# Kernel tuning notes

Measured on AMD Instinct MI355X. Metric: run time of the kernel, lower is better.

Reference implementation:

```python
import jax, jax.numpy as jnp
import numpy as np

TOP_K = 2
SCALING = 2.0  # LoRA alpha/rank scaling


def setup_inputs() -> dict:
    key = jax.random.key(0)
    ks = jax.random.split(key, 10)
    B, S, H, I, E, R = 1, 512, 2048, 1024, 8, 16
    w = 1.0 / np.sqrt(H)
    inp = {
        "x": jax.random.normal(ks[0], (B, S, H), jnp.float32),
        "gate_weight": jax.random.normal(ks[1], (E, H), jnp.float32) * w,
        "gate_lora_A": jax.random.normal(ks[2], (R, H), jnp.float32) * 0.02,
        "gate_lora_B": jax.random.normal(ks[3], (E, R), jnp.float32) * 0.02,
        "gate_up_proj": jax.random.normal(ks[4], (E, H, 2 * I), jnp.float32) * w,
        "down_proj": jax.random.normal(ks[5], (E, I, H), jnp.float32) * (1.0 / np.sqrt(I)),
        "gup_lora_A": jax.random.normal(ks[6], (E, R, H), jnp.float32) * 0.02,
        "gup_lora_B": jax.random.normal(ks[7], (E, 2 * I, R), jnp.float32) * 0.02,
        "down_lora_A": jax.random.normal(ks[8], (E, R, I), jnp.float32) * 0.02,
        "down_lora_B": jax.random.normal(ks[9], (E, H, R), jnp.float32) * 0.02,
    }
    return inp


def reference(x, gate_weight, gate_lora_A, gate_lora_B, gate_up_proj, down_proj,
              gup_lora_A, gup_lora_B, down_lora_A, down_lora_B):
    B, S, H = x.shape
    xf = x.reshape(-1, H)  # [T, H]

    # ---- router (base weight + LoRA delta) ----
    gate_delta = SCALING * (gate_lora_B @ gate_lora_A)  # [E, H]
    router_logits = xf @ gate_weight.T + xf @ gate_delta.T  # [T, E]
    probs = jax.nn.softmax(router_logits.astype(jnp.float32), axis=-1)
    routing_weights, selected = jax.lax.top_k(probs, TOP_K)  # [T, K]
    routing_weights = routing_weights / routing_weights.sum(-1, keepdims=True)  # norm_topk_prob
    routing_weights = routing_weights.astype(xf.dtype)

    # ---- expert MLP: compute all experts, combine top-k ----
    # (math identical to sparse scatter/grouped-GEMM dispatch for selected experts)
    gup = jnp.einsum('th,eho->teo', xf, gate_up_proj)  # [T, E, 2I]
    gup = gup + SCALING * jnp.einsum('ter,eor->teo',
                                     jnp.einsum('th,erh->ter', xf, gup_lora_A),
                                     gup_lora_B)
    gates, h = jnp.split(gup, 2, axis=-1)
    h = jax.nn.silu(gates) * h  # [T, E, I]

    out = jnp.einsum('tei,eih->teh', h, down_proj)  # [T, E, H]
    out = out + SCALING * jnp.einsum('ter,ehr->teh',
                                     jnp.einsum('tei,eri->ter', h, down_lora_A),
                                     down_lora_B)

    # gather the top-k expert outputs and combine with routing weights
    out_sel = jnp.take_along_axis(out, selected[:, :, None], axis=1)  # [T, K, H]
    y = jnp.einsum('tkh,tk->th', out_sel, routing_weights)
    return y.reshape(B, S, H)
```

## Files before the change

### kernel.cpp

```cpp
#include <hip/hip_runtime.h>


typedef short  s16x8 __attribute__((ext_vector_type(8)));
typedef float  f32x4 __attribute__((ext_vector_type(4)));
typedef unsigned short u16x8 __attribute__((ext_vector_type(8)));

__device__ __forceinline__ unsigned short f2bf(float f) {
  unsigned u = __builtin_bit_cast(unsigned, f);
  u += 0x7fffu + ((u >> 16) & 1u);
  return (unsigned short)(u >> 16);
}

#define PIPE_BARRIER() asm volatile("s_waitcnt lgkmcnt(0)\n\ts_barrier" ::: "memory")

#define OFF_CNT    0u
#define OFF_TER1A  256u
#define OFF_TER2   262400u
#define ZERO_SPAN  327936u
#define OFF_LIST   327936u
#define OFF_PW     344320u
#define OFF_WG     348416u
#define OFF_XBF    413952u
#define OFF_H      2511104u
#define OFF_OSEL   4608256u

__global__ void k_gatecomb(const float* __restrict__ gw, const float* __restrict__ gA,
                           const float* __restrict__ gB, float* __restrict__ Wg) {
  int idx = blockIdx.x * 256 + threadIdx.x;
  int e = idx >> 11, h = idx & 2047;
  float acc = gw[idx];
#pragma unroll
  for (int r = 0; r < 16; ++r)
    acc += 2.0f * gB[e * 16 + r] * gA[r * 2048 + h];
  Wg[idx] = acc;
}

__global__ void k_router(const float* __restrict__ x, const float* __restrict__ Wg,
                         int* __restrict__ cnt, int* __restrict__ list,
                         float* __restrict__ pw, unsigned short* __restrict__ xbf) {
  int t = blockIdx.x, tid = threadIdx.x;
  __shared__ float xs[2048];
  __shared__ float logits[8];
  for (int i = tid; i < 2048; i += 256) xs[i] = x[(size_t)t * 2048 + i];
  __syncthreads();
  {
    u16x8 o;
#pragma unroll
    for (int j = 0; j < 8; ++j) o[j] = f2bf(xs[tid * 8 + j]);
    *(u16x8*)(xbf + (size_t)t * 2048 + tid * 8) = o;
  }
  int e = tid >> 5, l = tid & 31;
  float s = 0.f;
  for (int h = l; h < 2048; h += 32) s += xs[h] * Wg[e * 2048 + h];
#pragma unroll
  for (int off = 16; off >= 1; off >>= 1) s += __shfl_down(s, off, 32);
  if (l == 0) logits[e] = s;
  __syncthreads();
  if (tid == 0) {
    float m = logits[0];
#pragma unroll
    for (int i = 1; i < 8; ++i) m = fmaxf(m, logits[i]);
    float ex[8];
#pragma unroll
    for (int i = 0; i < 8; ++i) ex[i] = __expf(logits[i] - m);
    int e1 = 0; float v1 = ex[0];
#pragma unroll
    for (int i = 1; i < 8; ++i) if (ex[i] > v1) { v1 = ex[i]; e1 = i; }
    int e2 = -1; float v2 = -1.f;
#pragma unroll
    for (int i = 0; i < 8; ++i) if (i != e1 && ex[i] > v2) { v2 = ex[i]; e2 = i; }
    float inv = 1.f / (v1 + v2);
    int p1 = 2 * t, p2 = 2 * t + 1;
    pw[p1] = v1 * inv;
    pw[p2] = v2 * inv;
    int s1 = atomicAdd(&cnt[e1], 1); list[e1 * 512 + s1] = p1;
    int s2 = atomicAdd(&cnt[e2], 1); list[e2 * 512 + s2] = p2;
  }
}

__global__ __launch_bounds__(512) void k_ter1all(
    const unsigned short* __restrict__ xbf, const float* __restrict__ gupA,
    float* __restrict__ ter1all) {
  int trow = blockIdx.x, kcc = blockIdx.y;
  int tid = threadIdx.x;
  __shared__ unsigned short Ap[2][64 * 64];
  __shared__ unsigned short Bp[2][128 * 64];
  const int k0b = kcc * 512;

  int rowA = tid >> 3, k16A = tid & 7;
  const unsigned short* aSrc = xbf + (size_t)(trow * 64 + rowA) * 2048 + k0b + k16A * 8;
  int aOff = rowA * 64 + ((k16A * 8) ^ ((rowA & 7) << 3));

  const float* bSrc[2]; int bOff[2];
#pragma unroll
  for (int s = 0; s < 2; ++s) {
    int slot = tid + s * 512;
    int er = slot >> 3, kg = slot & 7;
    bSrc[s] = gupA + (size_t)er * 2048 + k0b + kg * 8;
    bOff[s] = er * 64 + ((kg * 8) ^ ((er & 7) << 3));
  }
  int lane = tid & 63, wv = tid >> 6;
  int lr = lane & 15, lh = lane >> 4;

  uint4 apre; float4 bpre[2][2];
#define TA_ISSUE(T) { int kk = (T) * 64;                                   \
    apre = *(const uint4*)(aSrc + kk);                                     \
    _Pragma("unroll") for (int s = 0; s < 2; ++s) {                        \
      bpre[s][0] = *(const float4*)(bSrc[s] + kk);                         \
      bpre[s][1] = *(const float4*)(bSrc[s] + kk + 4); } }

  f32x4 acc[4] = {};
  TA_ISSUE(0);
  for (int t = 0; t < 8; ++t) {
    int buf = t & 1;
    *(uint4*)&Ap[buf][aOff] = apre;
#pragma unroll
    for (int s = 0; s < 2; ++s) {
      u16x8 o;
      o[0]=f2bf(bpre[s][0].x); o[1]=f2bf(bpre[s][0].y); o[2]=f2bf(bpre[s][0].z); o[3]=f2bf(bpre[s][0].w);
      o[4]=f2bf(bpre[s][1].x); o[5]=f2bf(bpre[s][1].y); o[6]=f2bf(bpre[s][1].z); o[7]=f2bf(bpre[s][1].w);
      *(u16x8*)&Bp[buf][bOff[s]] = o;
    }
    __syncthreads();
    if (t < 7) TA_ISSUE(t + 1);
#pragma unroll
    for (int ks = 0; ks < 64; ks += 32) {
      int kb = ks + lh * 8;
      int bc = wv * 16 + lr;
      s16x8 b = *(const s16x8*)&Bp[buf][bc * 64 + (kb ^ ((bc & 7) << 3))];
#pragma unroll
      for (int fr = 0; fr < 4; ++fr) {
        int ar = fr * 16 + lr;
        s16x8 a = *(const s16x8*)&Ap[buf][ar * 64 + (kb ^ ((ar & 7) << 3))];
        acc[fr] = __builtin_amdgcn_mfma_f32_16x16x32_bf16(a, b, acc[fr], 0, 0, 0);
      }
    }
    __syncthreads();
  }
#undef TA_ISSUE
#pragma unroll
  for (int fr = 0; fr < 4; ++fr)
#pragma unroll
    for (int j = 0; j < 4; ++j) {
      int tok = trow * 64 + fr * 16 + lh * 4 + j;
      atomicAdd(&ter1all[tok * 128 + wv * 16 + lr], acc[fr][j]);
    }
}

__global__ __launch_bounds__(512) void k_gemm1(
    const unsigned short* __restrict__ xbf, const float* __restrict__ gup,
    const float* __restrict__ gupB, const float* __restrict__ ter1all,
    const int* __restrict__ cnt, const int* __restrict__ list,
    unsigned short* __restrict__ h) {
  const int ct = blockIdx.x;
  const int st = blockIdx.y;
  const int e  = blockIdx.z;
  const int n = cnt[e];
  if (st * 128 >= n) return;
  const int tid = threadIdx.x;

  __shared__ unsigned short Ap[2][128 * 64];
  __shared__ unsigned short Bp[2][128 * 64];

  const int c0 = ct * 64;

  const unsigned short *aSrc0, *aSrc1;
  int aOff0, aOff1;
  {
    int row = tid >> 3, k16 = tid & 7;
    int p = list[e * 512 + min(st * 128 + row, n - 1)];
    aSrc0 = xbf + (size_t)(p >> 1) * 2048 + k16 * 8;
    aOff0 = row * 64 + ((k16 * 8) ^ ((row & 7) << 3));
    int slot = tid + 512;
    row = slot >> 3; k16 = slot & 7;
    p = list[e * 512 + min(st * 128 + row, n - 1)];
    aSrc1 = xbf + (size_t)(p >> 1) * 2048 + k16 * 8;
    aOff1 = row * 64 + ((k16 * 8) ^ ((row & 7) << 3));
  }
  const int bcol = tid & 127, kgrp = tid >> 7;
  const int gcg = (bcol < 64) ? (c0 + bcol) : (1024 + c0 + bcol - 64);
  const float* bSrc = gup + (size_t)e * 2048 * 2048 + (size_t)(kgrp * 16) * 2048 + gcg;
  const int sw = (bcol & 7) << 3;
  const int bOff0 = bcol * 64 + ((kgrp * 16) ^ sw);
  const int bOff1 = bcol * 64 + ((kgrp * 16 + 8) ^ sw);

  const int lane = tid & 63, wv = tid >> 6;
  const int lr = lane & 15, lh = lane >> 4;
  const int wr = wv >> 1, ni = wv & 1;

  uint4 a0A, a1A, a0B, a1B, a0C, a1C;
  float bA[16], bB[16], bC[16];

#define G1_LOAD(SUF, T) {                                        \
    const int kk = (T) * 64;                                     \
    a0##SUF = *(const uint4*)(aSrc0 + kk);                       \
    a1##SUF = *(const uint4*)(aSrc1 + kk);                       \
    _Pragma("unroll") for (int j = 0; j < 16; ++j)               \
      b##SUF[j] = bSrc[(size_t)(kk + j) * 2048]; }

#define G1_BODY(BUF, SUF, NXT) {                                               \
    *(uint4*)&Ap[BUF][aOff0] = a0##SUF;                                        \
    *(uint4*)&Ap[BUF][aOff1] = a1##SUF;                                        \
    { u16x8 o0, o1;                                                            \
      _Pragma("unroll") for (int j = 0; j < 8; ++j) {                          \
        o0[j] = f2bf(b##SUF[j]); o1[j] = f2bf(b##SUF[j + 8]); }                \
      *(u16x8*)&Bp[BUF][bOff0] = o0;                                           \
      *(u16x8*)&Bp[BUF][bOff1] = o1; }                                         \
    PIPE_BARRIER();                                                            \
    if ((NXT) < 32) G1_LOAD(SUF, NXT);                                         \
    _Pragma("unroll") for (int ks = 0; ks < 64; ks += 32) {                    \
      int kb = ks + lh * 8;                                                    \
      s16x8 af[2], bg[2], bu[2];                                               \
      _Pragma("unroll") for (int q = 0; q < 2; ++q) {                          \
        int ar = wr * 32 + q * 16 + lr;                                        \
        af[q] = *(const s16x8*)&Ap[BUF][ar * 64 + (kb ^ ((ar & 7) << 3))];     \
      }                                                                        \
      _Pragma("unroll") for (int r = 0; r < 2; ++r) {                          \
        int bc = ni * 32 + r * 16 + lr;                                        \
        bg[r] = *(const s16x8*)&Bp[BUF][bc * 64 + (kb ^ ((bc & 7) << 3))];     \
        bu[r] = *(const s16x8*)&Bp[BUF][(bc + 64) * 64 + (kb ^ ((bc & 7) << 3))]; \
      }                                                                        \
      _Pragma("unroll") for (int q = 0; q < 2; ++q)                            \
        _Pragma("unroll") for (int r = 0; r < 2; ++r) {                        \
          accg[q][r] = __builtin_amdgcn_mfma_f32_16x16x32_bf16(af[q], bg[r], accg[q][r], 0, 0, 0); \
          accu[q][r] = __builtin_amdgcn_mfma_f32_16x16x32_bf16(af[q], bu[r], accu[q][r], 0, 0, 0); \
        }                                                                      \
    } }

  f32x4 accg[2][2] = {}, accu[2][2] = {};
  G1_LOAD(A, 0);
  G1_LOAD(B, 1);
  G1_LOAD(C, 2);
  for (int tt = 0; tt < 30; tt += 6) {
    G1_BODY(0, A, tt + 3);
    G1_BODY(1, B, tt + 4);
    G1_BODY(0, C, tt + 5);
    G1_BODY(1, A, tt + 6);
    G1_BODY(0, B, tt + 7);
    G1_BODY(1, C, tt + 8);
  }
  G1_BODY(0, A, 99);
  G1_BODY(1, B, 99);
#undef G1_LOAD
#undef G1_BODY

  __syncthreads();
  float* tlds = (float*)&Ap[0][0];
  for (int idx = tid; idx < 2048; idx += 512) {
    int row = idx >> 4, c = idx & 15;
    int p = list[e * 512 + min(st * 128 + row, n - 1)];
    tlds[idx] = ter1all[(size_t)(p >> 1) * 128 + e * 16 + c];
  }
  __syncthreads();
#pragma unroll
  for (int r = 0; r < 2; ++r) {
    int gc = c0 + ni * 32 + r * 16 + lr;
    const float4* g4 = (const float4*)(gupB + ((size_t)e * 2048 + gc) * 16);
    const float4* u4 = (const float4*)(gupB + ((size_t)e * 2048 + 1024 + gc) * 16);
    float gv2[16], uv2[16];
#pragma unroll
    for (int q = 0; q < 4; ++q) {
      float4 gv = g4[q], uv = u4[q];
      gv2[q*4+0]=gv.x; gv2[q*4+1]=gv.y; gv2[q*4+2]=gv.z; gv2[q*4+3]=gv.w;
      uv2[q*4+0]=uv.x; uv2[q*4+1]=uv.y; uv2[q*4+2]=uv.z; uv2[q*4+3]=uv.w;
    }
#pragma unroll
    for (int q = 0; q < 2; ++q) {
#pragma unroll
      for (int j = 0; j < 4; ++j) {
        int row = wr * 32 + q * 16 + lh * 4 + j;
        if (st * 128 + row < n) {
          int p = list[e * 512 + st * 128 + row];
          const float* tv = &tlds[row * 16];
          float dg = 0.f, du = 0.f;
#pragma unroll
          for (int rr = 0; rr < 16; ++rr) { dg += tv[rr] * gv2[rr]; du += tv[rr] * uv2[rr]; }
          float g = accg[q][r][j] + 2.f * dg;
          float u = accu[q][r][j] + 2.f * du;
          h[(size_t)p * 1024 + gc] = f2bf(g / (1.f + __expf(-g)) * u);
        }
      }
    }
  }
}

__global__ __launch_bounds__(512) void k_ter2(
    const unsigned short* __restrict__ h, const float* __restrict__ dlA,
    const int* __restrict__ cnt, const int* __restrict__ list,
    float* __restrict__ ter2) {
  int st = blockIdx.x, kcc = blockIdx.y, e = blockIdx.z;
  int n = cnt[e];
  if (st * 128 >= n) return;
  int tid = threadIdx.x;
  __shared__ unsigned short Ap[2][128 * 64];
  __shared__ unsigned short Bp[2][16 * 64];
  const int k0b = kcc * 256;

  const unsigned short* aSrc[2]; int aOff[2];
#pragma unroll
  for (int s = 0; s < 2; ++s) {
    int slot = tid + s * 512;
    int row = slot >> 3, k16 = slot & 7;
    int p = list[e * 512 + min(st * 128 + row, n - 1)];
    aSrc[s] = h + (size_t)p * 1024 + k0b + k16 * 8;
    aOff[s] = row * 64 + ((k16 * 8) ^ ((row & 7) << 3));
  }
  const float* bSrc = nullptr; int bOff = 0;
  if (tid < 128) {
    int r = tid >> 3, kg = tid & 7;
    bSrc = dlA + ((size_t)e * 16 + r) * 1024 + k0b + kg * 8;
    bOff = r * 64 + ((kg * 8) ^ ((r & 7) << 3));
  }
  int lane = tid & 63, wv = tid >> 6;
  int lr = lane & 15, lh = lane >> 4;

  uint4 apre[2]; float4 bpre[2];
#define T2_ISSUE(T) { int kk = (T) * 64;                                   \
    _Pragma("unroll") for (int s = 0; s < 2; ++s)                          \
        apre[s] = *(const uint4*)(aSrc[s] + kk);                           \
    if (tid < 128) { bpre[0] = *(const float4*)(bSrc + kk);                \
                     bpre[1] = *(const float4*)(bSrc + kk + 4); } }

  f32x4 acc = {};
  T2_ISSUE(0);
  for (int t = 0; t < 4; ++t) {
    int buf = t & 1;
#pragma unroll
    for (int s = 0; s < 2; ++s) *(uint4*)&Ap[buf][aOff[s]] = apre[s];
    if (tid < 128) {
      u16x8 o;
      o[0]=f2bf(bpre[0].x); o[1]=f2bf(bpre[0].y); o[2]=f2bf(bpre[0].z); o[3]=f2bf(bpre[0].w);
      o[4]=f2bf(bpre[1].x); o[5]=f2bf(bpre[1].y); o[6]=f2bf(bpre[1].z); o[7]=f2bf(bpre[1].w);
      *(u16x8*)&Bp[buf][bOff] = o;
    }
    __syncthreads();
    if (t < 3) T2_ISSUE(t + 1);
#pragma unroll
    for (int ks = 0; ks < 64; ks += 32) {
      int kb = ks + lh * 8;
      s16x8 b = *(const s16x8*)&Bp[buf][lr * 64 + (kb ^ ((lr & 7) << 3))];
      int ar = wv * 16 + lr;
      s16x8 a = *(const s16x8*)&Ap[buf][ar * 64 + (kb ^ ((ar & 7) << 3))];
      acc = __builtin_amdgcn_mfma_f32_16x16x32_bf16(a, b, acc, 0, 0, 0);
    }
    __syncthreads();
  }
#undef T2_ISSUE
#pragma unroll
  for (int j = 0; j < 4; ++j) {
    int row = wv * 16 + lh * 4 + j;
    if (st * 128 + row < n) {
      int p = list[e * 512 + st * 128 + row];
      atomicAdd(&ter2[p * 16 + lr], acc[j]);
    }
  }
}

__global__ __launch_bounds__(512) void k_gemm2(
    const unsigned short* __restrict__ h, const float* __restrict__ down,
    const float* __restrict__ dlB, const float* __restrict__ ter2,
    const int* __restrict__ cnt, const int* __restrict__ list,
    float* __restrict__ osel) {
  const int ct = blockIdx.x;
  const int st = blockIdx.y;
  const int e  = blockIdx.z;
  const int n = cnt[e];
  if (st * 128 >= n) return;
  const int tid = threadIdx.x;

  __shared__ unsigned short Ap[2][128 * 64];
  __shared__ unsigned short Bp[2][64 * 64];

  const int c0 = ct * 64;

  const unsigned short *aSrc0, *aSrc1;
  int aOff0, aOff1;
  {
    int row = tid >> 3, k16 = tid & 7;
    int p = list[e * 512 + min(st * 128 + row, n - 1)];
    aSrc0 = h + (size_t)p * 1024 + k16 * 8;
    aOff0 = row * 64 + ((k16 * 8) ^ ((row & 7) << 3));
    int slot = tid + 512;
    row = slot >> 3; k16 = slot & 7;
    p = list[e * 512 + min(st * 128 + row, n - 1)];
    aSrc1 = h + (size_t)p * 1024 + k16 * 8;
    aOff1 = row * 64 + ((k16 * 8) ^ ((row & 7) << 3));
  }
  const int bcol = tid & 63, kg = tid >> 6;
  const float* bSrc = down + (size_t)e * 1024 * 2048 + (size_t)(kg * 8) * 2048 + c0 + bcol;
  const int bOff = bcol * 64 + ((kg * 8) ^ ((bcol & 7) << 3));

  const int lane = tid & 63, wv = tid >> 6;
  const int lr = lane & 15, lh = lane >> 4;
  const int wr = wv >> 1, ni = wv & 1;

  uint4 a0A, a1A, a0B, a1B, a0C, a1C;
  float bA[8], bB[8], bC[8];

#define G2_LOAD(SUF, T) {                                        \
    const int kk = (T) * 64;                                     \
    a0##SUF = *(const uint4*)(aSrc0 + kk);                       \
    a1##SUF = *(const uint4*)(aSrc1 + kk);                       \
    _Pragma("unroll") for (int j = 0; j < 8; ++j)                \
      b##SUF[j] = bSrc[(size_t)(kk + j) * 2048]; }

#define G2_BODY(BUF, SUF, NXT) {                                               \
    *(uint4*)&Ap[BUF][aOff0] = a0##SUF;                                        \
    *(uint4*)&Ap[BUF][aOff1] = a1##SUF;                                        \
    { u16x8 o;                                                                 \
      _Pragma("unroll") for (int j = 0; j < 8; ++j) o[j] = f2bf(b##SUF[j]);    \
      *(u16x8*)&Bp[BUF][bOff] = o; }                                           \
    PIPE_BARRIER();                                                            \
    if ((NXT) < 16) G2_LOAD(SUF, NXT);                                         \
    _Pragma("unroll") for (int ks = 0; ks < 64; ks += 32) {                    \
      int kb = ks + lh * 8;                                                    \
      s16x8 af[2], bd[2];                                                      \
      _Pragma("unroll") for (int q = 0; q < 2; ++q) {                          \
        int ar = wr * 32 + q * 16 + lr;                                        \
        af[q] = *(const s16x8*)&Ap[BUF][ar * 64 + (kb ^ ((ar & 7) << 3))];     \
      }                                                                        \
      _Pragma("unroll") for (int r = 0; r < 2; ++r) {                          \
        int bc = ni * 32 + r * 16 + lr;                                        \
        bd[r] = *(const s16x8*)&Bp[BUF][bc * 64 + (kb ^ ((bc & 7) << 3))];     \
      }                                                                        \
      _Pragma("unroll") for (int q = 0; q < 2; ++q)                            \
        _Pragma("unroll") for (int r = 0; r < 2; ++r)                          \
          acc[q][r] = __builtin_amdgcn_mfma_f32_16x16x32_bf16(af[q], bd[r], acc[q][r], 0, 0, 0); \
    } }

  f32x4 acc[2][2] = {};
  G2_LOAD(A, 0);
  G2_LOAD(B, 1);
  G2_LOAD(C, 2);
  for (int tt = 0; tt < 12; tt += 6) {
    G2_BODY(0, A, tt + 3);
    G2_BODY(1, B, tt + 4);
    G2_BODY(0, C, tt + 5);
    G2_BODY(1, A, tt + 6);
    G2_BODY(0, B, tt + 7);
    G2_BODY(1, C, tt + 8);
  }
  G2_BODY(0, A, 15);
  G2_BODY(1, B, 99);
  G2_BODY(0, C, 99);
  G2_BODY(1, A, 99);
#undef G2_LOAD
#undef G2_BODY

  __syncthreads();
  float* t2l = (float*)&Ap[0][0];
  for (int idx = tid; idx < 2048; idx += 512) {
    int row = idx >> 4, c = idx & 15;
    int p = list[e * 512 + min(st * 128 + row, n - 1)];
    t2l[idx] = ter2[p * 16 + c];
  }
  __syncthreads();
#pragma unroll
  for (int r = 0; r < 2; ++r) {
    int yc = c0 + ni * 32 + r * 16 + lr;
    const float4* d4 = (const float4*)(dlB + ((size_t)e * 2048 + yc) * 16);
    float d2[16];
#pragma unroll
    for (int q = 0; q < 4; ++q) {
      float4 v = d4[q];
      d2[q*4+0]=v.x; d2[q*4+1]=v.y; d2[q*4+2]=v.z; d2[q*4+3]=v.w;
    }
#pragma unroll
    for (int q = 0; q < 2; ++q) {
#pragma unroll
      for (int j = 0; j < 4; ++j) {
        int row = wr * 32 + q * 16 + lh * 4 + j;
        if (st * 128 + row < n) {
          int p = list[e * 512 + st * 128 + row];
          const float* tv = &t2l[row * 16];
          float dd = 0.f;
#pragma unroll
          for (int rr = 0; rr < 16; ++rr) dd += tv[rr] * d2[rr];
          osel[(size_t)p * 2048 + yc] = acc[q][r][j] + 2.f * dd;
        }
      }
    }
  }
}

__global__ __launch_bounds__(256) void k_comb(
    const float* __restrict__ osel, const float* __restrict__ pw,
    float* __restrict__ y) {
  int i = blockIdx.x * 256 + threadIdx.x;
  int t = i >> 9;
  int c4 = i & 511;
  float w1 = pw[2 * t], w2 = pw[2 * t + 1];
  const float4* o = (const float4*)osel;
  float4 a = o[(size_t)(2 * t) * 512 + c4];
  float4 b = o[(size_t)(2 * t + 1) * 512 + c4];
  float4 rv;
  rv.x = w1 * a.x + w2 * b.x;
  rv.y = w1 * a.y + w2 * b.y;
  rv.z = w1 * a.z + w2 * b.z;
  rv.w = w1 * a.w + w2 * b.w;
  ((float4*)y)[i] = rv;
}

extern "C" void kernel_launch(void* const* d_in, const int* in_sizes, int n_in,
                              void* d_out, int out_size, void* d_ws, size_t ws_size,
                              hipStream_t stream) {
  (void)in_sizes; (void)n_in; (void)ws_size; (void)out_size;
  const float* x    = (const float*)d_in[0];
  const float* gw   = (const float*)d_in[1];
  const float* gA   = (const float*)d_in[2];
  const float* gB   = (const float*)d_in[3];
  const float* gup  = (const float*)d_in[4];
  const float* down = (const float*)d_in[5];
  const float* gupA = (const float*)d_in[6];
  const float* gupB = (const float*)d_in[7];
  const float* dlA  = (const float*)d_in[8];
  const float* dlB  = (const float*)d_in[9];
  float* y = (float*)d_out;

  char* w = (char*)d_ws;
  int*   cnt           = (int*)(w + OFF_CNT);
  float* ter1all       = (float*)(w + OFF_TER1A);
  float* ter2          = (float*)(w + OFF_TER2);
  int*   list          = (int*)(w + OFF_LIST);
  float* pw            = (float*)(w + OFF_PW);
  float* Wg            = (float*)(w + OFF_WG);
  unsigned short* xbf  = (unsigned short*)(w + OFF_XBF);
  unsigned short* hbuf = (unsigned short*)(w + OFF_H);
  float* osel          = (float*)(w + OFF_OSEL);

  hipMemsetAsync(w, 0, ZERO_SPAN, stream);

  k_gatecomb<<<64, 256, 0, stream>>>(gw, gA, gB, Wg);
  k_router<<<512, 256, 0, stream>>>(x, Wg, cnt, list, pw, xbf);
  k_ter1all<<<dim3(8, 4), 512, 0, stream>>>(xbf, gupA, ter1all);
  k_gemm1<<<dim3(16, 4, 8), 512, 0, stream>>>(xbf, gup, gupB, ter1all, cnt, list, hbuf);
  k_ter2<<<dim3(4, 4, 8), 512, 0, stream>>>(hbuf, dlA, cnt, list, ter2);
  k_gemm2<<<dim3(32, 4, 8), 512, 0, stream>>>(hbuf, down, dlB, ter2, cnt, list, osel);
  k_comb<<<1024, 256, 0, stream>>>(osel, pw, y);
}
```

Before: 129.3 us.

## Fuse top-k combine into down GEMM epilogue and interleave expert block order

Removes the separate combine kernel and osel buffer. The down-projection GEMM now scales each output by its routing weight and accumulates directly into y with float atomics, after y is zeroed with a memset. Both grouped GEMMs also switch to a 1D grid with the expert index in the low bits, so blocks from different experts are spread across CUs and empty tiles are not clustered. This trades a launch and an extra read/write of osel for a memset and about 2M atomic adds. The atomics make the summation order of the two expert contributions nondeterministic.

Result: no change. 128.8 us (-0.4%).

```diff
diff --git a/kernel.cpp b/kernel.cpp
--- a/kernel.cpp
+++ b/kernel.cpp
@@ -22,7 +22,6 @@
 #define OFF_WG     348416u
 #define OFF_XBF    413952u
 #define OFF_H      2511104u
-#define OFF_OSEL   4608256u
 
 __global__ void k_gatecomb(const float* __restrict__ gw, const float* __restrict__ gA,
                            const float* __restrict__ gB, float* __restrict__ Wg) {
@@ -152,9 +151,11 @@
     const float* __restrict__ gupB, const float* __restrict__ ter1all,
     const int* __restrict__ cnt, const int* __restrict__ list,
     unsigned short* __restrict__ h) {
-  const int ct = blockIdx.x;
-  const int st = blockIdx.y;
-  const int e  = blockIdx.z;
+  const int id = blockIdx.x;
+  const int e  = id & 7;
+  const int m  = id >> 3;
+  const int ct = m & 15;
+  const int st = m >> 4;
   const int n = cnt[e];
   if (st * 128 >= n) return;
   const int tid = threadIdx.x;
@@ -360,10 +361,12 @@
     const unsigned short* __restrict__ h, const float* __restrict__ down,
     const float* __restrict__ dlB, const float* __restrict__ ter2,
     const int* __restrict__ cnt, const int* __restrict__ list,
-    float* __restrict__ osel) {
-  const int ct = blockIdx.x;
-  const int st = blockIdx.y;
-  const int e  = blockIdx.z;
+    const float* __restrict__ pw, float* __restrict__ y) {
+  const int id = blockIdx.x;
+  const int e  = id & 7;
+  const int m  = id >> 3;
+  const int ct = m & 31;
+  const int st = m >> 5;
   const int n = cnt[e];
   if (st * 128 >= n) return;
   const int tid = threadIdx.x;
@@ -476,35 +479,18 @@
           float dd = 0.f;
 #pragma unroll
           for (int rr = 0; rr < 16; ++rr) dd += tv[rr] * d2[rr];
-          osel[(size_t)p * 2048 + yc] = acc[q][r][j] + 2.f * dd;
+          atomicAdd(&y[(size_t)(p >> 1) * 2048 + yc],
+                    pw[p] * (acc[q][r][j] + 2.f * dd));
         }
       }
     }
   }
-}
-
-__global__ __launch_bounds__(256) void k_comb(
-    const float* __restrict__ osel, const float* __restrict__ pw,
-    float* __restrict__ y) {
-  int i = blockIdx.x * 256 + threadIdx.x;
-  int t = i >> 9;
-  int c4 = i & 511;
-  float w1 = pw[2 * t], w2 = pw[2 * t + 1];
-  const float4* o = (const float4*)osel;
-  float4 a = o[(size_t)(2 * t) * 512 + c4];
-  float4 b = o[(size_t)(2 * t + 1) * 512 + c4];
-  float4 rv;
-  rv.x = w1 * a.x + w2 * b.x;
-  rv.y = w1 * a.y + w2 * b.y;
-  rv.z = w1 * a.z + w2 * b.z;
-  rv.w = w1 * a.w + w2 * b.w;
-  ((float4*)y)[i] = rv;
 }
 
 extern "C" void kernel_launch(void* const* d_in, const int* in_sizes, int n_in,
                               void* d_out, int out_size, void* d_ws, size_t ws_size,
                               hipStream_t stream) {
-  (void)in_sizes; (void)n_in; (void)ws_size; (void)out_size;
+  (void)in_sizes; (void)n_in; (void)ws_size;
   const float* x    = (const float*)d_in[0];
   const float* gw   = (const float*)d_in[1];
   const float* gA   = (const float*)d_in[2];
@@ -526,15 +512,14 @@
   float* Wg            = (float*)(w + OFF_WG);
   unsigned short* xbf  = (unsigned short*)(w + OFF_XBF);
   unsigned short* hbuf = (unsigned short*)(w + OFF_H);
-  float* osel          = (float*)(w + OFF_OSEL);
 
   hipMemsetAsync(w, 0, ZERO_SPAN, stream);
+  hipMemsetAsync(y, 0, (size_t)out_size * sizeof(float), stream);
 
   k_gatecomb<<<64, 256, 0, stream>>>(gw, gA, gB, Wg);
   k_router<<<512, 256, 0, stream>>>(x, Wg, cnt, list, pw, xbf);
   k_ter1all<<<dim3(8, 4), 512, 0, stream>>>(xbf, gupA, ter1all);
-  k_gemm1<<<dim3(16, 4, 8), 512, 0, stream>>>(xbf, gup, gupB, ter1all, cnt, list, hbuf);
+  k_gemm1<<<512, 512, 0, stream>>>(xbf, gup, gupB, ter1all, cnt, list, hbuf);
   k_ter2<<<dim3(4, 4, 8), 512, 0, stream>>>(hbuf, dlA, cnt, list, ter2);
-  k_gemm2<<<dim3(32, 4, 8), 512, 0, stream>>>(hbuf, down, dlB, ter2, cnt, list, osel);
-  k_comb<<<1024, 256, 0, stream>>>(osel, pw, y);
-}
+  k_gemm2<<<1024, 512, 0, stream>>>(hbuf, down, dlB, ter2, cnt, list, pw, y);
+}
```
